# Optimization experiments

Measured on AMD Instinct MI355X. Metric: run time of the kernel, lower is better.

## Reference

```python
import jax, jax.numpy as jnp
import numpy as np

D_MODEL = 512
N_HEADS = 8
D_K = 64
B, T = 64, 256


def setup_inputs() -> dict:
    key = jax.random.key(0)
    ks = jax.random.split(key, 5)
    x = jax.random.normal(ks[0], (B, T, D_MODEL), dtype=jnp.float32)
    s = 1.0 / np.sqrt(D_MODEL)
    Wq = jax.random.normal(ks[1], (N_HEADS, D_MODEL, D_K), dtype=jnp.float32) * s
    Wk = jax.random.normal(ks[2], (N_HEADS, D_MODEL, D_K), dtype=jnp.float32) * s
    Wv = jax.random.normal(ks[3], (N_HEADS, D_MODEL, D_K), dtype=jnp.float32) * s
    Wo = jax.random.normal(ks[4], (N_HEADS * D_K, D_MODEL), dtype=jnp.float32) * s
    return {"x": x, "Wq": Wq, "Wk": Wk, "Wv": Wv, "Wo": Wo}


def reference(x, Wq, Wk, Wv, Wo):
    Bc, Tc, C = x.shape  # C == d_model; source scales by C**0.5, not sqrt(d_k)
    q = jnp.einsum('btc,hcd->bhtd', x, Wq)
    k = jnp.einsum('btc,hcd->bhtd', x, Wk)
    v = jnp.einsum('btc,hcd->bhtd', x, Wv)
    scores = jnp.einsum('bhtd,bhsd->bhts', q, k) / jnp.sqrt(jnp.float32(C))
    causal = jnp.tril(jnp.ones((Tc, Tc), dtype=bool))
    scores = jnp.where(causal, scores, -jnp.inf)
    attn = jax.nn.softmax(scores, axis=-1)  # dropout = identity in eval mode
    out = jnp.einsum('bhts,bhsd->bhtd', attn, v)
    out = out.transpose(0, 2, 1, 3).reshape(Bc, Tc, -1)  # concat heads
    return out @ Wo  # final dropout = identity in eval mode
```

## Files before the change

### kernel.cpp

```cpp
#include <hip/hip_runtime.h>
#include <hip/hip_bf16.h>

typedef __attribute__((ext_vector_type(4))) float f32x4;
typedef __attribute__((ext_vector_type(8))) short bf16x8;
typedef __attribute__((ext_vector_type(4))) short s16x4;
typedef __attribute__((ext_vector_type(4))) unsigned int u32x4;

#define DEV static __device__ __forceinline__

DEV unsigned short f2b(float f) {
  union { float f; unsigned int u; } v; v.f = f;
  unsigned int u = v.u;
  return (unsigned short)((u + 0x7fffu + ((u >> 16) & 1u)) >> 16);
}

DEV void gll16(const void* g, void* l) {
  __builtin_amdgcn_global_load_lds((__attribute__((address_space(1))) void*)g,
                                   (__attribute__((address_space(3))) void*)l,
                                   16, 0, 0);
}

__global__ __launch_bounds__(256) void prep(const float* __restrict__ x,
                                            const float* __restrict__ Wq,
                                            const float* __restrict__ Wk,
                                            const float* __restrict__ Wv,
                                            const float* __restrict__ Wo,
                                            unsigned short* __restrict__ xb,
                                            unsigned short* __restrict__ Wt,
                                            unsigned short* __restrict__ WoT) {
  int id = blockIdx.x * 256 + threadIdx.x;
  if (id < 2097152) {
    f32x4 v = *(const f32x4*)(x + (long)id * 4);
    s16x4 o;
    o.x = (short)f2b(v.x); o.y = (short)f2b(v.y);
    o.z = (short)f2b(v.z); o.w = (short)f2b(v.w);
    *(s16x4*)(xb + (long)id * 4) = o;
  } else {
    int j = id - 2097152;
    if (j < 786432) {
      int n = j >> 9, c = j & 511;
      int proj = n >> 9, hh = (n >> 6) & 7, d = n & 63;
      const float* W = (proj == 0) ? Wq : ((proj == 1) ? Wk : Wv);
      Wt[j] = f2b(W[hh * 32768 + c * 64 + d]);
    } else {
      int k = j - 786432;
      int n = k >> 9, c = k & 511;
      WoT[k] = f2b(Wo[c * 512 + n]);
    }
  }
}

template <int F32OUT>
__global__ __launch_bounds__(256, 2) void gemm_bt(const unsigned short* __restrict__ A,
                                                  const unsigned short* __restrict__ BT,
                                                  void* __restrict__ Cv,
                                                  int N) {
  const int K = 512;
  __shared__ unsigned short As[128 * 32];
  __shared__ unsigned short Bs[128 * 32];

  const int tid = threadIdx.x;
  const int wave = tid >> 6, lane = tid & 63;
  const int quad = lane >> 4, l16 = lane & 15;
  const int wm = wave >> 1, wn = wave & 1;
  const int bm = blockIdx.x, bn = blockIdx.y;

  const int srow = lane >> 2;
  const int scol = (lane & 3) * 8;

  f32x4 acc[4][4] = {};

  for (int kk = 0; kk < K; kk += 32) {
    __syncthreads();
#pragma unroll
    for (int it = 0; it < 2; it++) {
      int seg = wave * 2 + it;
      int row = seg * 16 + srow;
      gll16(A + (long)(bm * 128 + row) * K + kk + scol, As + seg * 512);
      gll16(BT + (long)(bn * 128 + row) * K + kk + scol, Bs + seg * 512);
    }
    __syncthreads();

    bf16x8 af[4], bfv[4];
#pragma unroll
    for (int mt = 0; mt < 4; mt++)
      af[mt] = *(const bf16x8*)(As + (wm * 64 + mt * 16 + l16) * 32 + quad * 8);
#pragma unroll
    for (int nt = 0; nt < 4; nt++)
      bfv[nt] = *(const bf16x8*)(Bs + (wn * 64 + nt * 16 + l16) * 32 + quad * 8);
#pragma unroll
    for (int mt = 0; mt < 4; mt++)
#pragma unroll
      for (int nt = 0; nt < 4; nt++)
        acc[mt][nt] = __builtin_amdgcn_mfma_f32_16x16x32_bf16(af[mt], bfv[nt], acc[mt][nt], 0, 0, 0);
  }

#pragma unroll
  for (int mt = 0; mt < 4; mt++) {
#pragma unroll
    for (int nt = 0; nt < 4; nt++) {
      int row0 = bm * 128 + wm * 64 + mt * 16 + quad * 4;
      int col = bn * 128 + wn * 64 + nt * 16 + l16;
      if (F32OUT) {
        float* cp = (float*)Cv + (long)row0 * N + col;
#pragma unroll
        for (int r = 0; r < 4; r++)
          cp[(long)r * N] = acc[mt][nt][r];
      } else {
        unsigned short* cp = (unsigned short*)Cv + (long)row0 * N + col;
#pragma unroll
        for (int r = 0; r < 4; r++)
          cp[(long)r * N] = f2b(acc[mt][nt][r]);
      }
    }
  }
}

__global__ __launch_bounds__(256, 2) void attn(const unsigned short* __restrict__ QKV,
                                               unsigned short* __restrict__ AO) {
  const int bh = blockIdx.x;
  const int b = bh >> 3, h = bh & 7;
  const int tid = threadIdx.x;
  const int wave = tid >> 6, lane = tid & 63;
  const int quad = lane >> 4, l16 = lane & 15;

  __shared__ unsigned short Kl[128 * 64];
  __shared__ unsigned short Vt[64 * 128];
  __shared__ unsigned short Pl[4][64 * 32];

  const unsigned short* Qb = QKV + (long)b * 256 * 1536 + h * 64;
  const unsigned short* Kb = Qb + 512;
  const unsigned short* Vb = Qb + 1024;

  bf16x8 qf[2][4];
#pragma unroll
  for (int kc = 0; kc < 2; kc++)
#pragma unroll
    for (int mt = 0; mt < 4; mt++)
      qf[kc][mt] = *(const bf16x8*)(Qb + (long)(wave * 64 + mt * 16 + l16) * 1536 + kc * 32 + quad * 8);

  f32x4 O[4][4] = {};
  float lsum[4][4] = {};
  const float scale = 0.044194173824159216f;

  for (int jc = 0; jc < 2; jc++) {
    __syncthreads();
#pragma unroll
    for (int p = 0; p < 4; p++) {
      int e = tid + 256 * p;
      int row = e >> 3, cg = e & 7;
      u32x4 d = *(const u32x4*)(Kb + (long)(jc * 128 + row) * 1536 + cg * 8);
      *(u32x4*)(Kl + row * 64 + cg * 8) = d;
    }
#pragma unroll
    for (int p = 0; p < 4; p++) {
      int e = tid + 256 * p;
      int j = e & 127, dg = e >> 7;
      union { u32x4 v; unsigned short s[8]; } d;
      d.v = *(const u32x4*)(Vb + (long)(jc * 128 + j) * 1536 + dg * 8);
#pragma unroll
      for (int q = 0; q < 8; q++) Vt[(dg * 8 + q) * 128 + j] = d.s[q];
    }
    __syncthreads();

    for (int s2 = 0; s2 < 2; s2++) {
      int sub = jc * 2 + s2;
      if (sub > wave) break;
      int jb = s2 * 64;
      bool diag = (sub == wave);
#pragma unroll
      for (int half = 0; half < 2; half++) {
        f32x4 S[4][2] = {};
#pragma unroll
        for (int kc = 0; kc < 2; kc++) {
          bf16x8 kbf[2];
#pragma unroll
          for (int st = 0; st < 2; st++)
            kbf[st] = *(const bf16x8*)(Kl + (jb + half * 32 + st * 16 + l16) * 64 + kc * 32 + quad * 8);
#pragma unroll
          for (int mt = 0; mt < 4; mt++)
#pragma unroll
            for (int st = 0; st < 2; st++)
              S[mt][st] = __builtin_amdgcn_mfma_f32_16x16x32_bf16(qf[kc][mt], kbf[st], S[mt][st], 0, 0, 0);
        }
#pragma unroll
        for (int mt = 0; mt < 4; mt++)
#pragma unroll
          for (int st = 0; st < 2; st++)
#pragma unroll
            for (int r = 0; r < 4; r++) {
              int trow = mt * 16 + quad * 4 + r;
              float p = __expf(S[mt][st][r] * scale);
              if (diag) {
                int scol = sub * 64 + half * 32 + st * 16 + l16;
                if (scol > wave * 64 + trow) p = 0.0f;
              }
              lsum[mt][r] += p;
              Pl[wave][trow * 32 + st * 16 + l16] = f2b(p);
            }
        bf16x8 pa[4], vbf[4];
#pragma unroll
        for (int mt = 0; mt < 4; mt++)
          pa[mt] = *(const bf16x8*)(&Pl[wave][(mt * 16 + l16) * 32 + quad * 8]);
#pragma unroll
        for (int dt = 0; dt < 4; dt++)
          vbf[dt] = *(const bf16x8*)(Vt + (dt * 16 + l16) * 128 + jb + half * 32 + quad * 8);
#pragma unroll
        for (int mt = 0; mt < 4; mt++)
#pragma unroll
          for (int dt = 0; dt < 4; dt++)
            O[mt][dt] = __builtin_amdgcn_mfma_f32_16x16x32_bf16(pa[mt], vbf[dt], O[mt][dt], 0, 0, 0);
      }
    }
  }

#pragma unroll
  for (int mt = 0; mt < 4; mt++)
#pragma unroll
    for (int r = 0; r < 4; r++) {
      float s = lsum[mt][r];
      s += __shfl_xor(s, 1); s += __shfl_xor(s, 2);
      s += __shfl_xor(s, 4); s += __shfl_xor(s, 8);
      lsum[mt][r] = 1.0f / s;
    }
#pragma unroll
  for (int mt = 0; mt < 4; mt++)
#pragma unroll
    for (int dt = 0; dt < 4; dt++)
#pragma unroll
      for (int r = 0; r < 4; r++) {
        int t = wave * 64 + mt * 16 + quad * 4 + r;
        int d = dt * 16 + l16;
        AO[(long)(b * 256 + t) * 512 + h * 64 + d] = f2b(O[mt][dt][r] * lsum[mt][r]);
      }
}

extern "C" void kernel_launch(void* const* d_in, const int* in_sizes, int n_in,
                              void* d_out, int out_size, void* d_ws, size_t ws_size,
                              hipStream_t stream) {
  const float* x  = (const float*)d_in[0];
  const float* Wq = (const float*)d_in[1];
  const float* Wk = (const float*)d_in[2];
  const float* Wv = (const float*)d_in[3];
  const float* Wo = (const float*)d_in[4];

  unsigned short* Wt  = (unsigned short*)d_ws;
  unsigned short* WoT = Wt + 1536 * 512;
  unsigned short* xb  = WoT + 512 * 512;
  unsigned short* QKV = xb + (long)16384 * 512;
  unsigned short* AO  = QKV + (long)16384 * 1536;
  float* out = (float*)d_out;

  prep<<<12288, 256, 0, stream>>>(x, Wq, Wk, Wv, Wo, xb, Wt, WoT);

  dim3 g1(128, 12);
  gemm_bt<0><<<g1, 256, 0, stream>>>(xb, Wt, (void*)QKV, 1536);

  attn<<<512, 256, 0, stream>>>(QKV, AO);

  dim3 g2(128, 4);
  gemm_bt<1><<<g2, 256, 0, stream>>>(AO, WoT, (void*)out, 512);
}
```

Baseline: 166.7 us.

## XOR-swizzle LDS layouts in GEMM and attention to remove bank conflicts

```diff
diff --git a/kernel.cpp b/kernel.cpp
--- a/kernel.cpp
+++ b/kernel.cpp
@@ -51,7 +51,7 @@
 }
 
 template <int F32OUT>
-__global__ __launch_bounds__(256, 2) void gemm_bt(const unsigned short* __restrict__ A,
+__global__ __launch_bounds__(256, 4) void gemm_bt(const unsigned short* __restrict__ A,
                                                   const unsigned short* __restrict__ BT,
                                                   void* __restrict__ Cv,
                                                   int N) {
@@ -66,7 +66,8 @@
   const int bm = blockIdx.x, bn = blockIdx.y;
 
   const int srow = lane >> 2;
-  const int scol = (lane & 3) * 8;
+  const int scol = (((lane & 3) ^ ((lane >> 3) & 3)) * 8);
+  const int rq = ((quad ^ ((l16 >> 1) & 3)) * 8);
 
   f32x4 acc[4][4] = {};
 
@@ -84,10 +85,10 @@
     bf16x8 af[4], bfv[4];
 #pragma unroll
     for (int mt = 0; mt < 4; mt++)
-      af[mt] = *(const bf16x8*)(As + (wm * 64 + mt * 16 + l16) * 32 + quad * 8);
+      af[mt] = *(const bf16x8*)(As + (wm * 64 + mt * 16 + l16) * 32 + rq);
 #pragma unroll
     for (int nt = 0; nt < 4; nt++)
-      bfv[nt] = *(const bf16x8*)(Bs + (wn * 64 + nt * 16 + l16) * 32 + quad * 8);
+      bfv[nt] = *(const bf16x8*)(Bs + (wn * 64 + nt * 16 + l16) * 32 + rq);
 #pragma unroll
     for (int mt = 0; mt < 4; mt++)
 #pragma unroll
@@ -150,16 +151,20 @@
       int e = tid + 256 * p;
       int row = e >> 3, cg = e & 7;
       u32x4 d = *(const u32x4*)(Kb + (long)(jc * 128 + row) * 1536 + cg * 8);
-      *(u32x4*)(Kl + row * 64 + cg * 8) = d;
+      *(u32x4*)(Kl + row * 64 + ((cg ^ (row & 7)) * 8)) = d;
     }
 #pragma unroll
     for (int p = 0; p < 4; p++) {
       int e = tid + 256 * p;
       int j = e & 127, dg = e >> 7;
+      int jg = j >> 3, jl = j & 7;
       union { u32x4 v; unsigned short s[8]; } d;
       d.v = *(const u32x4*)(Vb + (long)(jc * 128 + j) * 1536 + dg * 8);
 #pragma unroll
-      for (int q = 0; q < 8; q++) Vt[(dg * 8 + q) * 128 + j] = d.s[q];
+      for (int q = 0; q < 8; q++) {
+        int drow = dg * 8 + q;
+        Vt[drow * 128 + ((jg ^ (drow & 15)) << 3) + jl] = d.s[q];
+      }
     }
     __syncthreads();
 
@@ -175,8 +180,10 @@
         for (int kc = 0; kc < 2; kc++) {
           bf16x8 kbf[2];
 #pragma unroll
-          for (int st = 0; st < 2; st++)
-            kbf[st] = *(const bf16x8*)(Kl + (jb + half * 32 + st * 16 + l16) * 64 + kc * 32 + quad * 8);
+          for (int st = 0; st < 2; st++) {
+            int jrow = jb + half * 32 + st * 16 + l16;
+            kbf[st] = *(const bf16x8*)(Kl + jrow * 64 + (((kc * 4 + quad) ^ (jrow & 7)) * 8));
+          }
 #pragma unroll
           for (int mt = 0; mt < 4; mt++)
 #pragma unroll
@@ -196,15 +203,19 @@
                 if (scol > wave * 64 + trow) p = 0.0f;
               }
               lsum[mt][r] += p;
-              Pl[wave][trow * 32 + st * 16 + l16] = f2b(p);
+              int cgw = st * 2 + (l16 >> 3);
+              Pl[wave][trow * 32 + ((cgw ^ ((trow >> 1) & 3)) << 3) + (l16 & 7)] = f2b(p);
             }
         bf16x8 pa[4], vbf[4];
 #pragma unroll
         for (int mt = 0; mt < 4; mt++)
-          pa[mt] = *(const bf16x8*)(&Pl[wave][(mt * 16 + l16) * 32 + quad * 8]);
-#pragma unroll
-        for (int dt = 0; dt < 4; dt++)
-          vbf[dt] = *(const bf16x8*)(Vt + (dt * 16 + l16) * 128 + jb + half * 32 + quad * 8);
+          pa[mt] = *(const bf16x8*)(&Pl[wave][(mt * 16 + l16) * 32 + ((quad ^ ((l16 >> 1) & 3)) << 3)]);
+#pragma unroll
+        for (int dt = 0; dt < 4; dt++) {
+          int vrow = dt * 16 + l16;
+          int jg = (jb >> 3) + half * 4 + quad;
+          vbf[dt] = *(const bf16x8*)(Vt + vrow * 128 + ((jg ^ (vrow & 15)) << 3));
+        }
 #pragma unroll
         for (int mt = 0; mt < 4; mt++)
 #pragma unroll
```

Measured after the change: 185.8 us. 11.5% more time.

## Balance causal attention work across waves and swizzle GEMM LDS with deeper K tile

Applied to the files above, without the earlier changes.

```diff
diff --git a/kernel.cpp b/kernel.cpp
--- a/kernel.cpp
+++ b/kernel.cpp
@@ -56,8 +56,8 @@
                                                   void* __restrict__ Cv,
                                                   int N) {
   const int K = 512;
-  __shared__ unsigned short As[128 * 32];
-  __shared__ unsigned short Bs[128 * 32];
+  __shared__ unsigned short As[128 * 64];
+  __shared__ unsigned short Bs[128 * 64];
 
   const int tid = threadIdx.x;
   const int wave = tid >> 6, lane = tid & 63;
@@ -65,34 +65,38 @@
   const int wm = wave >> 1, wn = wave & 1;
   const int bm = blockIdx.x, bn = blockIdx.y;
 
-  const int srow = lane >> 2;
-  const int scol = (lane & 3) * 8;
+  const int srow = lane >> 3;
+  const int scol = ((lane & 7) ^ srow) * 8;
 
   f32x4 acc[4][4] = {};
 
-  for (int kk = 0; kk < K; kk += 32) {
+  for (int kk = 0; kk < K; kk += 64) {
     __syncthreads();
 #pragma unroll
-    for (int it = 0; it < 2; it++) {
-      int seg = wave * 2 + it;
-      int row = seg * 16 + srow;
+    for (int s = 0; s < 4; s++) {
+      int seg = wave * 4 + s;
+      int row = seg * 8 + srow;
       gll16(A + (long)(bm * 128 + row) * K + kk + scol, As + seg * 512);
       gll16(BT + (long)(bn * 128 + row) * K + kk + scol, Bs + seg * 512);
     }
     __syncthreads();
 
-    bf16x8 af[4], bfv[4];
-#pragma unroll
-    for (int mt = 0; mt < 4; mt++)
-      af[mt] = *(const bf16x8*)(As + (wm * 64 + mt * 16 + l16) * 32 + quad * 8);
-#pragma unroll
-    for (int nt = 0; nt < 4; nt++)
-      bfv[nt] = *(const bf16x8*)(Bs + (wn * 64 + nt * 16 + l16) * 32 + quad * 8);
-#pragma unroll
-    for (int mt = 0; mt < 4; mt++)
+#pragma unroll
+    for (int kc = 0; kc < 2; kc++) {
+      const int rq = (((kc * 4 + quad) ^ (l16 & 7)) * 8);
+      bf16x8 af[4], bfv[4];
+#pragma unroll
+      for (int mt = 0; mt < 4; mt++)
+        af[mt] = *(const bf16x8*)(As + (wm * 64 + mt * 16 + l16) * 64 + rq);
 #pragma unroll
       for (int nt = 0; nt < 4; nt++)
-        acc[mt][nt] = __builtin_amdgcn_mfma_f32_16x16x32_bf16(af[mt], bfv[nt], acc[mt][nt], 0, 0, 0);
+        bfv[nt] = *(const bf16x8*)(Bs + (wn * 64 + nt * 16 + l16) * 64 + rq);
+#pragma unroll
+      for (int mt = 0; mt < 4; mt++)
+#pragma unroll
+        for (int nt = 0; nt < 4; nt++)
+          acc[mt][nt] = __builtin_amdgcn_mfma_f32_16x16x32_bf16(af[mt], bfv[nt], acc[mt][nt], 0, 0, 0);
+    }
   }
 
 #pragma unroll
@@ -124,115 +128,122 @@
   const int wave = tid >> 6, lane = tid & 63;
   const int quad = lane >> 4, l16 = lane & 15;
 
-  __shared__ unsigned short Kl[128 * 64];
-  __shared__ unsigned short Vt[64 * 128];
-  __shared__ unsigned short Pl[4][64 * 32];
+  __shared__ unsigned short Kl[256 * 64];
+  __shared__ unsigned short Vt[64 * 264];
+  __shared__ unsigned short Pl[4][32 * 40];
 
   const unsigned short* Qb = QKV + (long)b * 256 * 1536 + h * 64;
   const unsigned short* Kb = Qb + 512;
   const unsigned short* Vb = Qb + 1024;
 
-  bf16x8 qf[2][4];
-#pragma unroll
-  for (int kc = 0; kc < 2; kc++)
-#pragma unroll
-    for (int mt = 0; mt < 4; mt++)
-      qf[kc][mt] = *(const bf16x8*)(Qb + (long)(wave * 64 + mt * 16 + l16) * 1536 + kc * 32 + quad * 8);
-
-  f32x4 O[4][4] = {};
-  float lsum[4][4] = {};
+  {
+    int r = lane >> 3, cg = lane & 7;
+#pragma unroll
+    for (int s = 0; s < 8; s++) {
+      int seg = wave * 8 + s;
+      gll16(Kb + (long)(seg * 8 + r) * 1536 + ((cg ^ r) * 8), Kl + seg * 512);
+    }
+  }
+  {
+    int j = tid;
+    const unsigned short* vp = Vb + (long)j * 1536;
+#pragma unroll
+    for (int g = 0; g < 8; g++) {
+      union { u32x4 v; unsigned short s[8]; } d;
+      d.v = *(const u32x4*)(vp + g * 8);
+#pragma unroll
+      for (int q = 0; q < 8; q++)
+        Vt[(g * 8 + q) * 264 + j] = d.s[q];
+    }
+  }
+  const int tiles[2] = {wave, 7 - wave};
+  bf16x8 qf[2][2][2];
+#pragma unroll
+  for (int ti = 0; ti < 2; ti++)
+#pragma unroll
+    for (int kc = 0; kc < 2; kc++)
+#pragma unroll
+      for (int mt = 0; mt < 2; mt++)
+        qf[ti][kc][mt] = *(const bf16x8*)(Qb +
+            (long)(tiles[ti] * 32 + mt * 16 + l16) * 1536 + kc * 32 + quad * 8);
+
+  __syncthreads();
+
+  f32x4 O[2][2][4] = {};
+  float lsum[2][2][4] = {};
   const float scale = 0.044194173824159216f;
 
-  for (int jc = 0; jc < 2; jc++) {
-    __syncthreads();
-#pragma unroll
-    for (int p = 0; p < 4; p++) {
-      int e = tid + 256 * p;
-      int row = e >> 3, cg = e & 7;
-      u32x4 d = *(const u32x4*)(Kb + (long)(jc * 128 + row) * 1536 + cg * 8);
-      *(u32x4*)(Kl + row * 64 + cg * 8) = d;
-    }
-#pragma unroll
-    for (int p = 0; p < 4; p++) {
-      int e = tid + 256 * p;
-      int j = e & 127, dg = e >> 7;
-      union { u32x4 v; unsigned short s[8]; } d;
-      d.v = *(const u32x4*)(Vb + (long)(jc * 128 + j) * 1536 + dg * 8);
-#pragma unroll
-      for (int q = 0; q < 8; q++) Vt[(dg * 8 + q) * 128 + j] = d.s[q];
-    }
-    __syncthreads();
-
-    for (int s2 = 0; s2 < 2; s2++) {
-      int sub = jc * 2 + s2;
-      if (sub > wave) break;
-      int jb = s2 * 64;
-      bool diag = (sub == wave);
-#pragma unroll
-      for (int half = 0; half < 2; half++) {
-        f32x4 S[4][2] = {};
-#pragma unroll
-        for (int kc = 0; kc < 2; kc++) {
-          bf16x8 kbf[2];
+#pragma unroll
+  for (int ti = 0; ti < 2; ti++) {
+    const int t = tiles[ti];
+    for (int c32 = 0; c32 <= t; c32++) {
+      f32x4 S[2][2] = {};
+#pragma unroll
+      for (int kc = 0; kc < 2; kc++) {
+        bf16x8 kbf[2];
+#pragma unroll
+        for (int st = 0; st < 2; st++) {
+          int jrow = c32 * 32 + st * 16 + l16;
+          kbf[st] = *(const bf16x8*)(Kl + jrow * 64 + (((kc * 4 + quad) ^ (jrow & 7)) * 8));
+        }
+#pragma unroll
+        for (int mt = 0; mt < 2; mt++)
 #pragma unroll
           for (int st = 0; st < 2; st++)
-            kbf[st] = *(const bf16x8*)(Kl + (jb + half * 32 + st * 16 + l16) * 64 + kc * 32 + quad * 8);
-#pragma unroll
-          for (int mt = 0; mt < 4; mt++)
-#pragma unroll
-            for (int st = 0; st < 2; st++)
-              S[mt][st] = __builtin_amdgcn_mfma_f32_16x16x32_bf16(qf[kc][mt], kbf[st], S[mt][st], 0, 0, 0);
+            S[mt][st] = __builtin_amdgcn_mfma_f32_16x16x32_bf16(qf[ti][kc][mt], kbf[st], S[mt][st], 0, 0, 0);
+      }
+      const bool diag = (c32 == t);
+#pragma unroll
+      for (int mt = 0; mt < 2; mt++)
+#pragma unroll
+        for (int st = 0; st < 2; st++)
+#pragma unroll
+          for (int r = 0; r < 4; r++) {
+            int trow = mt * 16 + quad * 4 + r;
+            float p = __expf(S[mt][st][r] * scale);
+            if (diag && (st * 16 + l16 > trow)) p = 0.0f;
+            lsum[ti][mt][r] += p;
+            Pl[wave][trow * 40 + st * 16 + l16] = f2b(p);
+          }
+      bf16x8 pa[2], vbf[4];
+#pragma unroll
+      for (int mt = 0; mt < 2; mt++)
+        pa[mt] = *(const bf16x8*)(&Pl[wave][(mt * 16 + l16) * 40 + quad * 8]);
+#pragma unroll
+      for (int dt = 0; dt < 4; dt++)
+        vbf[dt] = *(const bf16x8*)(Vt + (dt * 16 + l16) * 264 + c32 * 32 + quad * 8);
+#pragma unroll
+      for (int mt = 0; mt < 2; mt++)
+#pragma unroll
+        for (int dt = 0; dt < 4; dt++)
+          O[ti][mt][dt] = __builtin_amdgcn_mfma_f32_16x16x32_bf16(pa[mt], vbf[dt], O[ti][mt][dt], 0, 0, 0);
+    }
+  }
+
+  float linv[2][2][4];
+#pragma unroll
+  for (int ti = 0; ti < 2; ti++)
+#pragma unroll
+    for (int mt = 0; mt < 2; mt++)
+#pragma unroll
+      for (int r = 0; r < 4; r++) {
+        float s = lsum[ti][mt][r];
+        s += __shfl_xor(s, 1); s += __shfl_xor(s, 2);
+        s += __shfl_xor(s, 4); s += __shfl_xor(s, 8);
+        linv[ti][mt][r] = 1.0f / s;
+      }
+#pragma unroll
+  for (int ti = 0; ti < 2; ti++)
+#pragma unroll
+    for (int mt = 0; mt < 2; mt++)
+#pragma unroll
+      for (int dt = 0; dt < 4; dt++)
+#pragma unroll
+        for (int r = 0; r < 4; r++) {
+          int t_ = tiles[ti] * 32 + mt * 16 + quad * 4 + r;
+          int d = dt * 16 + l16;
+          AO[(long)(b * 256 + t_) * 512 + h * 64 + d] = f2b(O[ti][mt][dt][r] * linv[ti][mt][r]);
         }
-#pragma unroll
-        for (int mt = 0; mt < 4; mt++)
-#pragma unroll
-          for (int st = 0; st < 2; st++)
-#pragma unroll
-            for (int r = 0; r < 4; r++) {
-              int trow = mt * 16 + quad * 4 + r;
-              float p = __expf(S[mt][st][r] * scale);
-              if (diag) {
-                int scol = sub * 64 + half * 32 + st * 16 + l16;
-                if (scol > wave * 64 + trow) p = 0.0f;
-              }
-              lsum[mt][r] += p;
-              Pl[wave][trow * 32 + st * 16 + l16] = f2b(p);
-            }
-        bf16x8 pa[4], vbf[4];
-#pragma unroll
-        for (int mt = 0; mt < 4; mt++)
-          pa[mt] = *(const bf16x8*)(&Pl[wave][(mt * 16 + l16) * 32 + quad * 8]);
-#pragma unroll
-        for (int dt = 0; dt < 4; dt++)
-          vbf[dt] = *(const bf16x8*)(Vt + (dt * 16 + l16) * 128 + jb + half * 32 + quad * 8);
-#pragma unroll
-        for (int mt = 0; mt < 4; mt++)
-#pragma unroll
-          for (int dt = 0; dt < 4; dt++)
-            O[mt][dt] = __builtin_amdgcn_mfma_f32_16x16x32_bf16(pa[mt], vbf[dt], O[mt][dt], 0, 0, 0);
-      }
-    }
-  }
-
-#pragma unroll
-  for (int mt = 0; mt < 4; mt++)
-#pragma unroll
-    for (int r = 0; r < 4; r++) {
-      float s = lsum[mt][r];
-      s += __shfl_xor(s, 1); s += __shfl_xor(s, 2);
-      s += __shfl_xor(s, 4); s += __shfl_xor(s, 8);
-      lsum[mt][r] = 1.0f / s;
-    }
-#pragma unroll
-  for (int mt = 0; mt < 4; mt++)
-#pragma unroll
-    for (int dt = 0; dt < 4; dt++)
-#pragma unroll
-      for (int r = 0; r < 4; r++) {
-        int t = wave * 64 + mt * 16 + quad * 4 + r;
-        int d = dt * 16 + l16;
-        AO[(long)(b * 256 + t) * 512 + h * 64 + d] = f2b(O[mt][dt][r] * lsum[mt][r]);
-      }
 }
 
 extern "C" void kernel_launch(void* const* d_in, const int* in_sizes, int n_in,
```

Measured after the change: 154.9 us. 1.08x faster.
